# Optimization experiments

Hardware: AMD Instinct MI355X
Metric: run time of the kernel (lower is better)

## Reference

```python
import jax, jax.numpy as jnp
import numpy as np

B, T, N_EMBD, HEAD = 8, 2048, 1024, 64

def setup_inputs() -> dict:
    key = jax.random.key(0)
    kx, kk, kq, kv = jax.random.split(key, 4)
    x = jax.random.normal(kx, (B, T, N_EMBD), dtype=jnp.float32)
    Wk = jax.random.normal(kk, (HEAD, N_EMBD), dtype=jnp.float32) * 0.02
    Wq = jax.random.normal(kq, (HEAD, N_EMBD), dtype=jnp.float32) * 0.02
    Wv = jax.random.normal(kv, (HEAD, N_EMBD), dtype=jnp.float32) * 0.02
    return {"x": x, "Wk": Wk, "Wq": Wq, "Wv": Wv}

def reference(x, Wk, Wq, Wv):
    # x: [B, T, C]; Linear(n_embd, head_size, bias=False) => x @ W.T
    Bq, Tq, C = x.shape
    q = jnp.einsum('btc,hc->bth', x, Wq)  # [B, T, H]
    k = jnp.einsum('btc,hc->bth', x, Wk)
    v = jnp.einsum('btc,hc->bth', x, Wv)
    # NOTE: source scales by C**0.5 with C = n_embd (not head_size); preserved.
    scale = 1.0 / jnp.sqrt(jnp.float32(C))
    wei = jnp.einsum('bth,bsh->bts', q, k) * scale  # [B, T, T]
    # causal mask: allow key position s <= query position t
    causal = jnp.tril(jnp.ones((Tq, Tq), dtype=bool))
    wei = jnp.where(causal[None, :, :], wei, -jnp.inf)
    wei = jax.nn.softmax(wei, axis=-1)
    # dropout is identity at inference
    out = jnp.einsum('bts,bsh->bth', wei, v)  # [B, T, H]
    return out
```

## Files before the change

### kernel.cpp

```cpp
#include <hip/hip_runtime.h>

#define TB 2048
#define NB 8
#define CEMB 1024
#define HD 64
#define BT (NB*TB)
#define QSCALE 0.04508422f

typedef __attribute__((ext_vector_type(8))) short bf16x8;
typedef __attribute__((ext_vector_type(4))) float f32x4;

__device__ inline short f2bf(float f) {
    union { float f; unsigned u; } v; v.f = f;
    unsigned r = v.u + 0x7fffu + ((v.u >> 16) & 1u);
    return (short)(r >> 16);
}

__global__ __launch_bounds__(256) void wpack(const float* __restrict__ Wk,
                                             const float* __restrict__ Wq,
                                             const float* __restrict__ Wv,
                                             short* __restrict__ W2) {
    int c = blockIdx.x * 256 + threadIdx.x;
    int lane = c & 63, ntk = c >> 6;
    int nt = ntk % 12, kc = ntk / 12;
    int n = nt * 16 + (lane & 15);
    int col = kc * 32 + (lane >> 4) * 8;
    const float* src = (n < 64) ? Wk + n * 1024
                     : (n < 128) ? Wq + (n - 64) * 1024
                                 : Wv + (n - 128) * 1024;
    float4 a = *(const float4*)(src + col);
    float4 b = *(const float4*)(src + col + 4);
    bf16x8 o;
    o[0] = f2bf(a.x); o[1] = f2bf(a.y); o[2] = f2bf(a.z); o[3] = f2bf(a.w);
    o[4] = f2bf(b.x); o[5] = f2bf(b.y); o[6] = f2bf(b.z); o[7] = f2bf(b.w);
    *(bf16x8*)(W2 + (size_t)c * 8) = o;
}

__global__ __launch_bounds__(256, 3) void qkv_proj(const float* __restrict__ x,
                                                   const short* __restrict__ W2,
                                                   short* __restrict__ Qb,
                                                   short* __restrict__ Kb,
                                                   short* __restrict__ Vt) {
    __shared__ f32x4 Lred[4][3][3][64];
    int tid = threadIdx.x, wave = tid >> 6, lane = tid & 63;
    int l15 = lane & 15, quad = lane >> 4;
    int m0 = blockIdx.x * 16;
    int mrow = m0 + l15;

    f32x4 acc[12];
#pragma unroll
    for (int i = 0; i < 12; ++i) acc[i] = f32x4{0.f, 0.f, 0.f, 0.f};

    const float4* xb4 = (const float4*)(x + (size_t)mrow * CEMB + wave * 256) + quad * 2;
    float4 xr[16];
#pragma unroll
    for (int kc = 0; kc < 8; ++kc) {
        xr[2 * kc]     = xb4[kc * 8];
        xr[2 * kc + 1] = xb4[kc * 8 + 1];
    }

#pragma unroll
    for (int kc = 0; kc < 8; ++kc) {
        float4 x0 = xr[2 * kc], x1 = xr[2 * kc + 1];
        bf16x8 af;
        af[0] = f2bf(x0.x); af[1] = f2bf(x0.y); af[2] = f2bf(x0.z); af[3] = f2bf(x0.w);
        af[4] = f2bf(x1.x); af[5] = f2bf(x1.y); af[6] = f2bf(x1.z); af[7] = f2bf(x1.w);
        const short* wb = W2 + ((size_t)((wave * 8 + kc) * 12) * 64 + lane) * 8;
#pragma unroll
        for (int nt = 0; nt < 12; ++nt) {
            bf16x8 bf = *(const bf16x8*)(wb + nt * 512);
            acc[nt] = __builtin_amdgcn_mfma_f32_16x16x32_bf16(af, bf, acc[nt], 0, 0, 0);
        }
    }

#pragma unroll
    for (int nt = 0; nt < 12; ++nt) {
        int o = nt / 3;
        if (o != wave) {
            int rank = wave - (wave > o ? 1 : 0);
            Lred[o][rank][nt % 3][lane] = acc[nt];
        }
    }
    __syncthreads();

    int b = blockIdx.x >> 7;
    int sblk = (m0 & 2047) >> 4;
#pragma unroll
    for (int nt = 0; nt < 12; ++nt) {
        if (wave == nt / 3) {
            f32x4 s = acc[nt];
#pragma unroll
            for (int rk = 0; rk < 3; ++rk) s += Lred[nt / 3][rk][nt % 3][lane];
            if (nt < 4) {
                int h = nt * 16 + l15;
#pragma unroll
                for (int r = 0; r < 4; ++r)
                    Kb[(size_t)(m0 + quad * 4 + r) * HD + h] = f2bf(s[r]);
            } else if (nt < 8) {
                int h = (nt - 4) * 16 + l15;
#pragma unroll
                for (int r = 0; r < 4; ++r)
                    Qb[(size_t)(m0 + quad * 4 + r) * HD + h] = f2bf(s[r] * QSCALE);
            } else {
                int h = (nt - 8) * 16 + l15;
                short4 o4;
                o4.x = f2bf(s[0]); o4.y = f2bf(s[1]); o4.z = f2bf(s[2]); o4.w = f2bf(s[3]);
                *(short4*)(Vt + ((size_t)(b * 128 + sblk) * 64 + h) * 16 + quad * 4) = o4;
            }
        }
    }
}

#define PPAD 72
__global__ __launch_bounds__(256) void flash(const short* __restrict__ Qb,
                                             const short* __restrict__ Kb,
                                             const short* __restrict__ Vt,
                                             float* __restrict__ out) {
    __shared__ short U[4][2432];
    __shared__ float Ml[4][16];
    int tid = threadIdx.x, wave = tid >> 6, lane = tid & 63;
    int l15 = lane & 15, quad = lane >> 4;
    int i = blockIdx.x;
    int round = i >> 8, s = i & 255;
    int b = round * 2 + (s & 1);
    int q = (round & 1) ? 127 - (s >> 1) : (s >> 1);
    int tq0 = q * 16;
    size_t bT = (size_t)b * TB;

    const short* qrow = Qb + (bT + tq0 + l15) * HD;
    bf16x8 qf0 = *(const bf16x8*)(qrow + quad * 8);
    bf16x8 qf1 = *(const bf16x8*)(qrow + 32 + quad * 8);

    f32x4 accO[4];
#pragma unroll
    for (int k = 0; k < 4; ++k) accO[k] = f32x4{0.f, 0.f, 0.f, 0.f};
    float lrow[4] = {0.f, 0.f, 0.f, 0.f};

    int ntiles = (q + 4) >> 2;
    const short* kbase = Kb + bT * HD;
    const short* vtb = Vt + (size_t)b * 131072;
    short* Psh = U[wave];

    int myt = wave;
    if (myt < ntiles) {
        bf16x8 kf[8];
        {
            const short* kr = kbase + (size_t)(myt * 64 + l15) * HD + quad * 8;
#pragma unroll
            for (int st = 0; st < 4; ++st) {
                kf[st * 2]     = *(const bf16x8*)(kr + (size_t)st * 16 * HD);
                kf[st * 2 + 1] = *(const bf16x8*)(kr + (size_t)st * 16 * HD + 32);
            }
        }
        for (; myt < ntiles; myt += 4) {
            int s0 = myt * 64;
            bf16x8 vf[8];
            {
                int sb = (s0 >> 4) + (quad >> 1);
                int so = (quad & 1) * 8;
#pragma unroll
                for (int ht = 0; ht < 4; ++ht) {
                    vf[ht * 2]     = *(const bf16x8*)(vtb + (sb * 64 + ht * 16 + l15) * 16 + so);
                    vf[ht * 2 + 1] = *(const bf16x8*)(vtb + ((sb + 2) * 64 + ht * 16 + l15) * 16 + so);
                }
            }
            f32x4 sv[4];
#pragma unroll
            for (int st = 0; st < 4; ++st) {
                f32x4 sacc = f32x4{0.f, 0.f, 0.f, 0.f};
                sacc = __builtin_amdgcn_mfma_f32_16x16x32_bf16(qf0, kf[st * 2], sacc, 0, 0, 0);
                sacc = __builtin_amdgcn_mfma_f32_16x16x32_bf16(qf1, kf[st * 2 + 1], sacc, 0, 0, 0);
                sv[st] = sacc;
            }
            if (myt + 4 < ntiles) {
                const short* kr = kbase + (size_t)(s0 + 256 + l15) * HD + quad * 8;
#pragma unroll
                for (int st = 0; st < 4; ++st) {
                    kf[st * 2]     = *(const bf16x8*)(kr + (size_t)st * 16 * HD);
                    kf[st * 2 + 1] = *(const bf16x8*)(kr + (size_t)st * 16 * HD + 32);
                }
            }
            bool full = (s0 + 64 <= tq0);
#pragma unroll
            for (int r = 0; r < 4; ++r) {
                int tg = tq0 + quad * 4 + r;
                float e0, e1, e2, e3;
                if (full) {
                    e0 = __builtin_amdgcn_exp2f(sv[0][r]);
                    e1 = __builtin_amdgcn_exp2f(sv[1][r]);
                    e2 = __builtin_amdgcn_exp2f(sv[2][r]);
                    e3 = __builtin_amdgcn_exp2f(sv[3][r]);
                } else {
                    int sg = s0 + l15;
                    e0 = (sg      <= tg) ? __builtin_amdgcn_exp2f(sv[0][r]) : 0.f;
                    e1 = (sg + 16 <= tg) ? __builtin_amdgcn_exp2f(sv[1][r]) : 0.f;
                    e2 = (sg + 32 <= tg) ? __builtin_amdgcn_exp2f(sv[2][r]) : 0.f;
                    e3 = (sg + 48 <= tg) ? __builtin_amdgcn_exp2f(sv[3][r]) : 0.f;
                }
                float rs = (e0 + e1) + (e2 + e3);
                rs += __shfl_xor(rs, 1);
                rs += __shfl_xor(rs, 2);
                rs += __shfl_xor(rs, 4);
                rs += __shfl_xor(rs, 8);
                lrow[r] += rs;
                int prow = (quad * 4 + r) * PPAD;
                Psh[prow + l15]      = f2bf(e0);
                Psh[prow + 16 + l15] = f2bf(e1);
                Psh[prow + 32 + l15] = f2bf(e2);
                Psh[prow + 48 + l15] = f2bf(e3);
            }
            asm volatile("s_waitcnt lgkmcnt(0)" ::: "memory");
            bf16x8 pf0 = *(const bf16x8*)&Psh[l15 * PPAD + quad * 8];
            bf16x8 pf1 = *(const bf16x8*)&Psh[l15 * PPAD + 32 + quad * 8];
#pragma unroll
            for (int ht = 0; ht < 4; ++ht) {
                accO[ht] = __builtin_amdgcn_mfma_f32_16x16x32_bf16(pf0, vf[ht * 2], accO[ht], 0, 0, 0);
                accO[ht] = __builtin_amdgcn_mfma_f32_16x16x32_bf16(pf1, vf[ht * 2 + 1], accO[ht], 0, 0, 0);
            }
        }
    }

    float* of = (float*)U[wave];
#pragma unroll
    for (int ht = 0; ht < 4; ++ht)
#pragma unroll
        for (int r = 0; r < 4; ++r)
            of[(quad * 4 + r) * 68 + ht * 16 + l15] = accO[ht][r];
    if (l15 == 0) {
#pragma unroll
        for (int r = 0; r < 4; ++r)
            Ml[wave][quad * 4 + r] = lrow[r];
    }
    __syncthreads();

    int row = tid >> 4, c4 = (tid & 15) * 4;
    float L = Ml[0][row] + Ml[1][row] + Ml[2][row] + Ml[3][row];
    float inv = 1.0f / L;
    float4 p0 = *(const float4*)((const float*)U[0] + row * 68 + c4);
    float4 p1 = *(const float4*)((const float*)U[1] + row * 68 + c4);
    float4 p2 = *(const float4*)((const float*)U[2] + row * 68 + c4);
    float4 p3 = *(const float4*)((const float*)U[3] + row * 68 + c4);
    float4 o;
    o.x = (p0.x + p1.x + p2.x + p3.x) * inv;
    o.y = (p0.y + p1.y + p2.y + p3.y) * inv;
    o.z = (p0.z + p1.z + p2.z + p3.z) * inv;
    o.w = (p0.w + p1.w + p2.w + p3.w) * inv;
    *(float4*)(out + (bT + tq0 + row) * HD + c4) = o;
}

extern "C" void kernel_launch(void* const* d_in, const int* in_sizes, int n_in,
                              void* d_out, int out_size, void* d_ws, size_t ws_size,
                              hipStream_t stream) {
    const float* x  = (const float*)d_in[0];
    const float* Wk = (const float*)d_in[1];
    const float* Wq = (const float*)d_in[2];
    const float* Wv = (const float*)d_in[3];
    float* out = (float*)d_out;

    short* W2 = (short*)d_ws;
    short* Qb = W2 + 192 * 1024;
    short* Kb = Qb + (size_t)BT * HD;
    short* Vt = Kb + (size_t)BT * HD;

    wpack<<<96, 256, 0, stream>>>(Wk, Wq, Wv, W2);
    qkv_proj<<<1024, 256, 0, stream>>>(x, W2, Qb, Kb, Vt);
    flash<<<1024, 256, 0, stream>>>(Qb, Kb, Vt, out);
}
```

Baseline: 149.9 us.

## Compute softmax row sums via MFMA with ones, hoist weight loads, bf16 LDS reduction

In the attention kernel, the per-row softmax denominator is now accumulated with two extra MFMAs against a ones vector, using the same bf16 P fragments. This replaces the four cross-lane shuffle reductions per row and sums the same rounded values used for P·V. In the projection kernel, the 12 weight loads per k-chunk are issued before the MFMAs and a sched barrier is added. The cross-wave partial sums are also stored in LDS as bf16 rather than fp32, halving LDS traffic and dropping the occupancy hint, at some precision cost for Q/K/V.

```diff
diff --git a/kernel.cpp b/kernel.cpp
--- a/kernel.cpp
+++ b/kernel.cpp
@@ -14,6 +14,10 @@
     union { float f; unsigned u; } v; v.f = f;
     unsigned r = v.u + 0x7fffu + ((v.u >> 16) & 1u);
     return (short)(r >> 16);
+}
+__device__ inline float bf2f(short s) {
+    union { unsigned u; float f; } v; v.u = ((unsigned)(unsigned short)s) << 16;
+    return v.f;
 }
 
 __global__ __launch_bounds__(256) void wpack(const float* __restrict__ Wk,
@@ -36,12 +40,12 @@
     *(bf16x8*)(W2 + (size_t)c * 8) = o;
 }
 
-__global__ __launch_bounds__(256, 3) void qkv_proj(const float* __restrict__ x,
-                                                   const short* __restrict__ W2,
-                                                   short* __restrict__ Qb,
-                                                   short* __restrict__ Kb,
-                                                   short* __restrict__ Vt) {
-    __shared__ f32x4 Lred[4][3][3][64];
+__global__ __launch_bounds__(256) void qkv_proj(const float* __restrict__ x,
+                                                const short* __restrict__ W2,
+                                                short* __restrict__ Qb,
+                                                short* __restrict__ Kb,
+                                                short* __restrict__ Vt) {
+    __shared__ short4 Lred[4][3][3][64];
     int tid = threadIdx.x, wave = tid >> 6, lane = tid & 63;
     int l15 = lane & 15, quad = lane >> 4;
     int m0 = blockIdx.x * 16;
@@ -58,19 +62,22 @@
         xr[2 * kc]     = xb4[kc * 8];
         xr[2 * kc + 1] = xb4[kc * 8 + 1];
     }
+    __builtin_amdgcn_sched_barrier(0);
 
 #pragma unroll
     for (int kc = 0; kc < 8; ++kc) {
+        const short* wb = W2 + ((size_t)((wave * 8 + kc) * 12) * 64 + lane) * 8;
+        bf16x8 wf[12];
+#pragma unroll
+        for (int nt = 0; nt < 12; ++nt)
+            wf[nt] = *(const bf16x8*)(wb + nt * 512);
         float4 x0 = xr[2 * kc], x1 = xr[2 * kc + 1];
         bf16x8 af;
         af[0] = f2bf(x0.x); af[1] = f2bf(x0.y); af[2] = f2bf(x0.z); af[3] = f2bf(x0.w);
         af[4] = f2bf(x1.x); af[5] = f2bf(x1.y); af[6] = f2bf(x1.z); af[7] = f2bf(x1.w);
-        const short* wb = W2 + ((size_t)((wave * 8 + kc) * 12) * 64 + lane) * 8;
-#pragma unroll
-        for (int nt = 0; nt < 12; ++nt) {
-            bf16x8 bf = *(const bf16x8*)(wb + nt * 512);
-            acc[nt] = __builtin_amdgcn_mfma_f32_16x16x32_bf16(af, bf, acc[nt], 0, 0, 0);
-        }
+#pragma unroll
+        for (int nt = 0; nt < 12; ++nt)
+            acc[nt] = __builtin_amdgcn_mfma_f32_16x16x32_bf16(af, wf[nt], acc[nt], 0, 0, 0);
     }
 
 #pragma unroll
@@ -78,7 +85,10 @@
         int o = nt / 3;
         if (o != wave) {
             int rank = wave - (wave > o ? 1 : 0);
-            Lred[o][rank][nt % 3][lane] = acc[nt];
+            short4 p;
+            p.x = f2bf(acc[nt][0]); p.y = f2bf(acc[nt][1]);
+            p.z = f2bf(acc[nt][2]); p.w = f2bf(acc[nt][3]);
+            Lred[o][rank][nt % 3][lane] = p;
         }
     }
     __syncthreads();
@@ -90,7 +100,11 @@
         if (wave == nt / 3) {
             f32x4 s = acc[nt];
 #pragma unroll
-            for (int rk = 0; rk < 3; ++rk) s += Lred[nt / 3][rk][nt % 3][lane];
+            for (int rk = 0; rk < 3; ++rk) {
+                short4 p = Lred[nt / 3][rk][nt % 3][lane];
+                s[0] += bf2f(p.x); s[1] += bf2f(p.y);
+                s[2] += bf2f(p.z); s[3] += bf2f(p.w);
+            }
             if (nt < 4) {
                 int h = nt * 16 + l15;
 #pragma unroll
@@ -131,10 +145,14 @@
     bf16x8 qf0 = *(const bf16x8*)(qrow + quad * 8);
     bf16x8 qf1 = *(const bf16x8*)(qrow + 32 + quad * 8);
 
+    bf16x8 onesf;
+#pragma unroll
+    for (int j = 0; j < 8; ++j) onesf[j] = (short)0x3F80;
+
     f32x4 accO[4];
 #pragma unroll
     for (int k = 0; k < 4; ++k) accO[k] = f32x4{0.f, 0.f, 0.f, 0.f};
-    float lrow[4] = {0.f, 0.f, 0.f, 0.f};
+    f32x4 accL = f32x4{0.f, 0.f, 0.f, 0.f};
 
     int ntiles = (q + 4) >> 2;
     const short* kbase = Kb + bT * HD;
@@ -197,12 +215,6 @@
                     e2 = (sg + 32 <= tg) ? __builtin_amdgcn_exp2f(sv[2][r]) : 0.f;
                     e3 = (sg + 48 <= tg) ? __builtin_amdgcn_exp2f(sv[3][r]) : 0.f;
                 }
-                float rs = (e0 + e1) + (e2 + e3);
-                rs += __shfl_xor(rs, 1);
-                rs += __shfl_xor(rs, 2);
-                rs += __shfl_xor(rs, 4);
-                rs += __shfl_xor(rs, 8);
-                lrow[r] += rs;
                 int prow = (quad * 4 + r) * PPAD;
                 Psh[prow + l15]      = f2bf(e0);
                 Psh[prow + 16 + l15] = f2bf(e1);
@@ -212,6 +224,8 @@
             asm volatile("s_waitcnt lgkmcnt(0)" ::: "memory");
             bf16x8 pf0 = *(const bf16x8*)&Psh[l15 * PPAD + quad * 8];
             bf16x8 pf1 = *(const bf16x8*)&Psh[l15 * PPAD + 32 + quad * 8];
+            accL = __builtin_amdgcn_mfma_f32_16x16x32_bf16(pf0, onesf, accL, 0, 0, 0);
+            accL = __builtin_amdgcn_mfma_f32_16x16x32_bf16(pf1, onesf, accL, 0, 0, 0);
 #pragma unroll
             for (int ht = 0; ht < 4; ++ht) {
                 accO[ht] = __builtin_amdgcn_mfma_f32_16x16x32_bf16(pf0, vf[ht * 2], accO[ht], 0, 0, 0);
@@ -229,7 +243,7 @@
     if (l15 == 0) {
 #pragma unroll
         for (int r = 0; r < 4; ++r)
-            Ml[wave][quad * 4 + r] = lrow[r];
+            Ml[wave][quad * 4 + r] = accL[r];
     }
     __syncthreads();
 
```

Result: faster. 146.3 us (-2.4%).
